# Kernel tuning notes

Hardware: AMD Instinct MI355X
Metric: run time of the kernel (lower is better)

Reference implementation:

```python
import jax, jax.numpy as jnp
import numpy as np

N, C, T, H, W = 4, 512, 8, 28, 28
CQ, CV = C // 8, C // 2  # 64, 256


def _maxpool222(a):
    # max_pool3d with kernel=stride=(2,2,2), VALID, over (t,h,w) of [n,c,t,h,w]
    return jax.lax.reduce_window(a, -jnp.inf, jax.lax.max,
                                 (1, 1, 2, 2, 2), (1, 1, 2, 2, 2), 'VALID')


def setup_inputs() -> dict:
    key = jax.random.key(0)
    ks = jax.random.split(key, 6)
    s = lambda fan_in: 1.0 / np.sqrt(fan_in)
    return {
        'x':  jax.random.normal(ks[0], (N, C, T, H, W), dtype=jnp.float32),
        'Wq': jax.random.normal(ks[1], (CQ, C), dtype=jnp.float32) * s(C),
        'Wk': jax.random.normal(ks[2], (CQ, C), dtype=jnp.float32) * s(C),
        'Wv': jax.random.normal(ks[3], (CV, C), dtype=jnp.float32) * s(C),
        'Wz': jax.random.normal(ks[4], (C, CV), dtype=jnp.float32) * s(CV),
        'y':  jax.random.normal(ks[5], (), dtype=jnp.float32) * 0.1,
    }


def reference(x, Wq, Wk, Wv, Wz, y):
    n, c, t, h, w = x.shape
    # 1x1x1 convs (no bias) = per-voxel channel mixing
    q = jnp.einsum('ncthw,oc->nothw', x, Wq)          # [n, CQ, t, h, w]
    k = _maxpool222(jnp.einsum('ncthw,oc->nothw', x, Wk))  # [n, CQ, t/2, h/2, w/2]
    v = _maxpool222(jnp.einsum('ncthw,oc->nothw', x, Wv))  # [n, CV, t/2, h/2, w/2]

    Lq = t * h * w
    Lk = k.shape[2] * k.shape[3] * k.shape[4]
    qf = q.reshape(n, q.shape[1], Lq)                 # [n, CQ, Lq]
    kf = k.reshape(n, k.shape[1], Lk)                 # [n, CQ, Lk]
    vf = v.reshape(n, v.shape[1], Lk)                 # [n, CV, Lk]

    # beta = softmax(q^T k) over kv axis (NOTE: no 1/sqrt(d) scaling, as in source)
    beta = jax.nn.softmax(jnp.einsum('ncq,nck->nqk', qf, kf), axis=-1)  # [n, Lq, Lk]
    att = jnp.einsum('nck,nqk->ncq', vf, beta)        # [n, CV, Lq]
    att = att.reshape(n, vf.shape[1], t, h, w)

    z = jnp.einsum('ncthw,oc->nothw', att, Wz)        # [n, C, t, h, w]
    return y * z + x
```

## Files before the change

kernel.cpp:

```cpp
#include <hip/hip_runtime.h>
#include <hip/hip_bf16.h>

#define LSP  6272
#define LK   784
#define CIN  512
#define CQo  64
#define CVo  256
#define NB   4

typedef __bf16  bf16x8 __attribute__((ext_vector_type(8)));
typedef __bf16  bf16x4 __attribute__((ext_vector_type(4)));
typedef float   f32x4  __attribute__((ext_vector_type(4)));

#define LDT  40
#define LDS2 72

__global__ __launch_bounds__(256) void xt_kernel(const float* __restrict__ x,
                                                 __bf16* __restrict__ xT)
{
    __shared__ __attribute__((aligned(16))) __bf16 tile[64][68];
    int t = threadIdx.x;
    int p0 = blockIdx.x * 64, c0 = blockIdx.y * 64, n = blockIdx.z;
    #pragma unroll
    for (int i = 0; i < 4; i++) {
        int idx = i * 256 + t;
        int c = idx >> 4, p4 = (idx & 15) * 4;
        const float4 v = *reinterpret_cast<const float4*>(
            &x[((size_t)(n * CIN + c0 + c)) * LSP + p0 + p4]);
        tile[p4 + 0][c] = (__bf16)v.x;
        tile[p4 + 1][c] = (__bf16)v.y;
        tile[p4 + 2][c] = (__bf16)v.z;
        tile[p4 + 3][c] = (__bf16)v.w;
    }
    __syncthreads();
    #pragma unroll
    for (int i = 0; i < 4; i++) {
        int idx = i * 256 + t;
        int p = idx >> 4, c4 = (idx & 15) * 4;
        bf16x4 o;
        o[0] = tile[p][c4 + 0]; o[1] = tile[p][c4 + 1];
        o[2] = tile[p][c4 + 2]; o[3] = tile[p][c4 + 3];
        *reinterpret_cast<bf16x4*>(&xT[((size_t)(n * LSP + p0 + p)) * CIN + c0 + c4]) = o;
    }
}

__global__ void wprep_kernel(const float* __restrict__ Wq, const float* __restrict__ Wk,
                             const float* __restrict__ Wv, const float* __restrict__ Wz,
                             __bf16* __restrict__ Wqkv, __bf16* __restrict__ Wzb)
{
    int idx = blockIdx.x * 256 + threadIdx.x;
    if (idx < 384 * 512) {
        int o = idx >> 9;
        float v = (o < 64) ? Wq[idx] : (o < 128) ? Wk[idx - 64 * 512] : Wv[idx - 128 * 512];
        Wqkv[idx] = (__bf16)v;
    }
    if (idx < 512 * 256) Wzb[idx] = (__bf16)Wz[idx];
}

__global__ __launch_bounds__(256) void qkv_gemm(const __bf16* __restrict__ Wqkv,
                                                const __bf16* __restrict__ xT,
                                                __bf16* __restrict__ qT,
                                                __bf16* __restrict__ kT,
                                                __bf16* __restrict__ vconv)
{
    __shared__ __attribute__((aligned(16))) __bf16 As[128 * LDT];
    __shared__ __attribute__((aligned(16))) __bf16 Bs[128 * LDT];
    int t = threadIdx.x;
    int p0 = blockIdx.x * 128;
    int m0 = blockIdx.y * 128;
    int n  = blockIdx.z;
    int lane = t & 63, wid = t >> 6;
    int wm = wid >> 1, wn = wid & 1;
    int lm = lane & 15, lk = lane >> 4;

    f32x4 acc[4][4] = {};

    for (int kb = 0; kb < CIN; kb += 32) {
        #pragma unroll
        for (int i = 0; i < 2; i++) {
            int idx = i * 2048 + t * 8;
            int r = idx >> 5, k8 = idx & 31;
            uint4 va = *reinterpret_cast<const uint4*>(&Wqkv[(size_t)(m0 + r) * CIN + kb + k8]);
            *reinterpret_cast<uint4*>(&As[r * LDT + k8]) = va;
            uint4 vb = *reinterpret_cast<const uint4*>(&xT[((size_t)(n * LSP + p0 + r)) * CIN + kb + k8]);
            *reinterpret_cast<uint4*>(&Bs[r * LDT + k8]) = vb;
        }
        __syncthreads();
        bf16x8 a[4], b[4];
        #pragma unroll
        for (int mi = 0; mi < 4; mi++)
            a[mi] = *reinterpret_cast<const bf16x8*>(&As[(wm * 64 + mi * 16 + lm) * LDT + lk * 8]);
        #pragma unroll
        for (int ni = 0; ni < 4; ni++)
            b[ni] = *reinterpret_cast<const bf16x8*>(&Bs[(wn * 64 + ni * 16 + lm) * LDT + lk * 8]);
        #pragma unroll
        for (int mi = 0; mi < 4; mi++)
            #pragma unroll
            for (int ni = 0; ni < 4; ni++)
                acc[mi][ni] = __builtin_amdgcn_mfma_f32_16x16x32_bf16(a[mi], b[ni], acc[mi][ni], 0, 0, 0);
        __syncthreads();
    }

    #pragma unroll
    for (int mi = 0; mi < 4; mi++) {
        int mloc = wm * 64 + mi * 16 + lk * 4;
        #pragma unroll
        for (int ni = 0; ni < 4; ni++) {
            int p = p0 + wn * 64 + ni * 16 + lm;
            if (m0 == 0) {
                bf16x4 o;
                o[0] = (__bf16)acc[mi][ni][0]; o[1] = (__bf16)acc[mi][ni][1];
                o[2] = (__bf16)acc[mi][ni][2]; o[3] = (__bf16)acc[mi][ni][3];
                if (mloc < 64)
                    *reinterpret_cast<bf16x4*>(&qT[((size_t)(n * LSP + p)) * 64 + mloc]) = o;
                else
                    *reinterpret_cast<bf16x4*>(&kT[((size_t)(n * LSP + p)) * 64 + (mloc - 64)]) = o;
            } else {
                int cv = m0 - 128 + mloc;
                #pragma unroll
                for (int r = 0; r < 4; r++)
                    vconv[((size_t)(n * CVo + cv + r)) * LSP + p] = (__bf16)acc[mi][ni][r];
            }
        }
    }
}

__global__ __launch_bounds__(256) void poolk_kernel(const __bf16* __restrict__ kT,
                                                    __bf16* __restrict__ kpT)
{
    int wid = threadIdx.x >> 6, lane = threadIdx.x & 63;
    int row = blockIdx.x * 4 + wid;
    int n = row / LK, pk = row % LK;
    int tp = pk / 196, rem = pk % 196, hp = rem / 14, wp = rem % 14;
    const __bf16* b = kT + ((size_t)n * LSP + tp * 2 * 784 + hp * 2 * 28 + wp * 2) * 64 + lane;
    float m =        (float)b[0];
    m = fmaxf(m, (float)b[64]);
    m = fmaxf(m, (float)b[28 * 64]);
    m = fmaxf(m, (float)b[29 * 64]);
    m = fmaxf(m, (float)b[784 * 64]);
    m = fmaxf(m, (float)b[785 * 64]);
    m = fmaxf(m, (float)b[812 * 64]);
    m = fmaxf(m, (float)b[813 * 64]);
    kpT[(size_t)row * 64 + lane] = (__bf16)m;
}

__global__ void poolv_kernel(const __bf16* __restrict__ vconv, __bf16* __restrict__ vp)
{
    int id = blockIdx.x * 256 + threadIdx.x;
    if (id >= NB * CVo * LK) return;
    int nc = id / LK, pk = id % LK;
    int tp = pk / 196, rem = pk % 196, hp = rem / 14, wp = rem % 14;
    const __bf16* b = vconv + (size_t)nc * LSP + tp * 2 * 784 + hp * 2 * 28 + wp * 2;
    float m =        (float)b[0];
    m = fmaxf(m, (float)b[1]);   m = fmaxf(m, (float)b[28]);  m = fmaxf(m, (float)b[29]);
    m = fmaxf(m, (float)b[784]); m = fmaxf(m, (float)b[785]); m = fmaxf(m, (float)b[812]); m = fmaxf(m, (float)b[813]);
    vp[id] = (__bf16)m;
}

__global__ __launch_bounds__(256) void scores_gemm(const __bf16* __restrict__ qT,
                                                   const __bf16* __restrict__ kpT,
                                                   __bf16* __restrict__ sc)
{
    __shared__ __attribute__((aligned(16))) __bf16 As[128 * LDS2];
    __shared__ __attribute__((aligned(16))) __bf16 Bs[128 * LDS2];
    int t = threadIdx.x;
    int k0 = blockIdx.x * 128;
    int q0 = blockIdx.y * 128;
    int n  = blockIdx.z;
    int lane = t & 63, wid = t >> 6;
    int wm = wid >> 1, wn = wid & 1;
    int lm = lane & 15, lk = lane >> 4;

    #pragma unroll
    for (int i = 0; i < 4; i++) {
        int idx = i * 2048 + t * 8;
        int r = idx >> 6, k8 = idx & 63;
        *reinterpret_cast<uint4*>(&As[r * LDS2 + k8]) =
            *reinterpret_cast<const uint4*>(&qT[((size_t)(n * LSP + q0 + r)) * 64 + k8]);
        uint4 vb = {0u, 0u, 0u, 0u};
        if (k0 + r < LK)
            vb = *reinterpret_cast<const uint4*>(&kpT[((size_t)(n * LK + k0 + r)) * 64 + k8]);
        *reinterpret_cast<uint4*>(&Bs[r * LDS2 + k8]) = vb;
    }
    __syncthreads();

    f32x4 acc[4][4] = {};
    #pragma unroll
    for (int ks = 0; ks < 2; ks++) {
        bf16x8 a[4], b[4];
        #pragma unroll
        for (int mi = 0; mi < 4; mi++)
            a[mi] = *reinterpret_cast<const bf16x8*>(&As[(wm * 64 + mi * 16 + lm) * LDS2 + ks * 32 + lk * 8]);
        #pragma unroll
        for (int ni = 0; ni < 4; ni++)
            b[ni] = *reinterpret_cast<const bf16x8*>(&Bs[(wn * 64 + ni * 16 + lm) * LDS2 + ks * 32 + lk * 8]);
        #pragma unroll
        for (int mi = 0; mi < 4; mi++)
            #pragma unroll
            for (int ni = 0; ni < 4; ni++)
                acc[mi][ni] = __builtin_amdgcn_mfma_f32_16x16x32_bf16(a[mi], b[ni], acc[mi][ni], 0, 0, 0);
    }

    #pragma unroll
    for (int mi = 0; mi < 4; mi++) {
        int q = q0 + wm * 64 + mi * 16 + lk * 4;
        #pragma unroll
        for (int ni = 0; ni < 4; ni++) {
            int k = k0 + wn * 64 + ni * 16 + lm;
            if (k < LK) {
                #pragma unroll
                for (int r = 0; r < 4; r++)
                    sc[((size_t)(n * LSP + q + r)) * LK + k] = (__bf16)acc[mi][ni][r];
            }
        }
    }
}

__global__ __launch_bounds__(256) void softmax_kernel(__bf16* __restrict__ sc)
{
    int wid = threadIdx.x >> 6, lane = threadIdx.x & 63;
    size_t row = (size_t)blockIdx.x * 4 + wid;
    __bf16* r = sc + row * LK;
    float v[13];
    float mx = -1e30f;
    #pragma unroll
    for (int i = 0; i < 13; i++) {
        int k = lane + i * 64;
        v[i] = (k < LK) ? (float)r[k] : -1e30f;
        mx = fmaxf(mx, v[i]);
    }
    #pragma unroll
    for (int s = 32; s > 0; s >>= 1) mx = fmaxf(mx, __shfl_xor(mx, s));
    float sum = 0.0f;
    #pragma unroll
    for (int i = 0; i < 13; i++) {
        float e = (lane + i * 64 < LK) ? __expf(v[i] - mx) : 0.0f;
        v[i] = e;
        sum += e;
    }
    #pragma unroll
    for (int s = 32; s > 0; s >>= 1) sum += __shfl_xor(sum, s);
    float inv = 1.0f / sum;
    #pragma unroll
    for (int i = 0; i < 13; i++) {
        int k = lane + i * 64;
        if (k < LK) r[k] = (__bf16)(v[i] * inv);
    }
}

__global__ __launch_bounds__(256) void pv_gemm(const __bf16* __restrict__ vp,
                                               const __bf16* __restrict__ sc,
                                               __bf16* __restrict__ attT)
{
    __shared__ __attribute__((aligned(16))) __bf16 As[128 * LDT];
    __shared__ __attribute__((aligned(16))) __bf16 Bs[128 * LDT];
    int t = threadIdx.x;
    int q0 = blockIdx.x * 128;
    int m0 = blockIdx.y * 128;
    int n  = blockIdx.z;
    int lane = t & 63, wid = t >> 6;
    int wm = wid >> 1, wn = wid & 1;
    int lm = lane & 15, lk = lane >> 4;

    f32x4 acc[4][4] = {};

    for (int kb = 0; kb < 800; kb += 32) {
        #pragma unroll
        for (int i = 0; i < 2; i++) {
            int idx = i * 2048 + t * 8;
            int r = idx >> 5, k8 = idx & 31;
            uint4 va = {0u, 0u, 0u, 0u}, vb = {0u, 0u, 0u, 0u};
            if (kb + k8 < LK) {
                va = *reinterpret_cast<const uint4*>(&vp[((size_t)(n * CVo + m0 + r)) * LK + kb + k8]);
                vb = *reinterpret_cast<const uint4*>(&sc[((size_t)(n * LSP + q0 + r)) * LK + kb + k8]);
            }
            *reinterpret_cast<uint4*>(&As[r * LDT + k8]) = va;
            *reinterpret_cast<uint4*>(&Bs[r * LDT + k8]) = vb;
        }
        __syncthreads();
        bf16x8 a[4], b[4];
        #pragma unroll
        for (int mi = 0; mi < 4; mi++)
            a[mi] = *reinterpret_cast<const bf16x8*>(&As[(wm * 64 + mi * 16 + lm) * LDT + lk * 8]);
        #pragma unroll
        for (int ni = 0; ni < 4; ni++)
            b[ni] = *reinterpret_cast<const bf16x8*>(&Bs[(wn * 64 + ni * 16 + lm) * LDT + lk * 8]);
        #pragma unroll
        for (int mi = 0; mi < 4; mi++)
            #pragma unroll
            for (int ni = 0; ni < 4; ni++)
                acc[mi][ni] = __builtin_amdgcn_mfma_f32_16x16x32_bf16(a[mi], b[ni], acc[mi][ni], 0, 0, 0);
        __syncthreads();
    }

    #pragma unroll
    for (int mi = 0; mi < 4; mi++) {
        int cvb = m0 + wm * 64 + mi * 16 + lk * 4;
        #pragma unroll
        for (int ni = 0; ni < 4; ni++) {
            int q = q0 + wn * 64 + ni * 16 + lm;
            bf16x4 o;
            o[0] = (__bf16)acc[mi][ni][0]; o[1] = (__bf16)acc[mi][ni][1];
            o[2] = (__bf16)acc[mi][ni][2]; o[3] = (__bf16)acc[mi][ni][3];
            *reinterpret_cast<bf16x4*>(&attT[((size_t)(n * LSP + q)) * CVo + cvb]) = o;
        }
    }
}

__global__ __launch_bounds__(256) void z_gemm(const __bf16* __restrict__ Wzb,
                                              const __bf16* __restrict__ attT,
                                              const float* __restrict__ x,
                                              const float* __restrict__ yp,
                                              float* __restrict__ out)
{
    __shared__ __attribute__((aligned(16))) __bf16 As[128 * LDT];
    __shared__ __attribute__((aligned(16))) __bf16 Bs[128 * LDT];
    int t = threadIdx.x;
    int p0 = blockIdx.x * 128;
    int m0 = blockIdx.y * 128;
    int n  = blockIdx.z;
    int lane = t & 63, wid = t >> 6;
    int wm = wid >> 1, wn = wid & 1;
    int lm = lane & 15, lk = lane >> 4;

    f32x4 acc[4][4] = {};

    for (int kb = 0; kb < CVo; kb += 32) {
        #pragma unroll
        for (int i = 0; i < 2; i++) {
            int idx = i * 2048 + t * 8;
            int r = idx >> 5, k8 = idx & 31;
            uint4 va = *reinterpret_cast<const uint4*>(&Wzb[(size_t)(m0 + r) * CVo + kb + k8]);
            *reinterpret_cast<uint4*>(&As[r * LDT + k8]) = va;
            uint4 vb = *reinterpret_cast<const uint4*>(&attT[((size_t)(n * LSP + p0 + r)) * CVo + kb + k8]);
            *reinterpret_cast<uint4*>(&Bs[r * LDT + k8]) = vb;
        }
        __syncthreads();
        bf16x8 a[4], b[4];
        #pragma unroll
        for (int mi = 0; mi < 4; mi++)
            a[mi] = *reinterpret_cast<const bf16x8*>(&As[(wm * 64 + mi * 16 + lm) * LDT + lk * 8]);
        #pragma unroll
        for (int ni = 0; ni < 4; ni++)
            b[ni] = *reinterpret_cast<const bf16x8*>(&Bs[(wn * 64 + ni * 16 + lm) * LDT + lk * 8]);
        #pragma unroll
        for (int mi = 0; mi < 4; mi++)
            #pragma unroll
            for (int ni = 0; ni < 4; ni++)
                acc[mi][ni] = __builtin_amdgcn_mfma_f32_16x16x32_bf16(a[mi], b[ni], acc[mi][ni], 0, 0, 0);
        __syncthreads();
    }

    float yv = yp[0];
    #pragma unroll
    for (int mi = 0; mi < 4; mi++) {
        int c = m0 + wm * 64 + mi * 16 + lk * 4;
        #pragma unroll
        for (int ni = 0; ni < 4; ni++) {
            int p = p0 + wn * 64 + ni * 16 + lm;
            #pragma unroll
            for (int r = 0; r < 4; r++) {
                size_t o = ((size_t)(n * CIN + c + r)) * LSP + p;
                out[o] = yv * acc[mi][ni][r] + x[o];
            }
        }
    }
}

extern "C" void kernel_launch(void* const* d_in, const int* in_sizes, int n_in,
                              void* d_out, int out_size, void* d_ws, size_t ws_size,
                              hipStream_t stream)
{
    const float* x  = (const float*)d_in[0];
    const float* Wq = (const float*)d_in[1];
    const float* Wk = (const float*)d_in[2];
    const float* Wv = (const float*)d_in[3];
    const float* Wz = (const float*)d_in[4];
    const float* y  = (const float*)d_in[5];
    float* out = (float*)d_out;
    __bf16* ws = (__bf16*)d_ws;

    __bf16* xT    = ws;
    __bf16* kT    = ws + (size_t)12845056;
    __bf16* vconv = ws + (size_t)14450688;
    __bf16* sc    = ws;
    __bf16* qT    = ws + (size_t)20873216;
    __bf16* kpT   = ws + (size_t)22478848;
    __bf16* vp    = ws + (size_t)22679552;
    __bf16* attT  = ws + (size_t)23482368;
    __bf16* Wqkv  = ws + (size_t)29904896;
    __bf16* Wzb   = ws + (size_t)30101504;

    xt_kernel   <<<dim3(98, 8, 4), 256, 0, stream>>>(x, xT);
    wprep_kernel<<<dim3(768), 256, 0, stream>>>(Wq, Wk, Wv, Wz, Wqkv, Wzb);
    qkv_gemm    <<<dim3(49, 3, 4), 256, 0, stream>>>(Wqkv, xT, qT, kT, vconv);
    poolk_kernel<<<dim3(784), 256, 0, stream>>>(kT, kpT);
    poolv_kernel<<<dim3(3136), 256, 0, stream>>>(vconv, vp);
    scores_gemm <<<dim3(7, 49, 4), 256, 0, stream>>>(qT, kpT, sc);
    softmax_kernel<<<dim3(6272), 256, 0, stream>>>(sc);
    pv_gemm     <<<dim3(49, 2, 4), 256, 0, stream>>>(vp, sc, attT);
    z_gemm      <<<dim3(49, 4, 4), 256, 0, stream>>>(Wzb, attT, x, y, out);
}
```

Before: 247.4 us.

## Fuse scores, softmax and PV into a flash-attention kernel; vectorize z epilogue

Replaces the separate scores GEMM, softmax pass and PV GEMM with a single online-softmax flash kernel that keeps the probability tile in LDS, so the full 6272x784 score matrix is never written to or re-read from global memory. Each 64-query block streams K and V tiles straight from global memory without LDS staging and rescales its accumulators per tile. The z GEMM operands are also swapped so the epilogue writes float4 along the spatial axis, giving coalesced reads of x and writes of out. The flash grid is small (392 blocks), and the unstaged K/V global loads may limit MFMA throughput.

```diff
diff --git a/kernel.cpp b/kernel.cpp
--- a/kernel.cpp
+++ b/kernel.cpp
@@ -13,7 +13,6 @@
 typedef float   f32x4  __attribute__((ext_vector_type(4)));
 
 #define LDT  40
-#define LDS2 72
 
 __global__ __launch_bounds__(256) void xt_kernel(const float* __restrict__ x,
                                                  __bf16* __restrict__ xT)
@@ -80,10 +79,10 @@
         for (int i = 0; i < 2; i++) {
             int idx = i * 2048 + t * 8;
             int r = idx >> 5, k8 = idx & 31;
-            uint4 va = *reinterpret_cast<const uint4*>(&Wqkv[(size_t)(m0 + r) * CIN + kb + k8]);
-            *reinterpret_cast<uint4*>(&As[r * LDT + k8]) = va;
-            uint4 vb = *reinterpret_cast<const uint4*>(&xT[((size_t)(n * LSP + p0 + r)) * CIN + kb + k8]);
-            *reinterpret_cast<uint4*>(&Bs[r * LDT + k8]) = vb;
+            *reinterpret_cast<uint4*>(&As[r * LDT + k8]) =
+                *reinterpret_cast<const uint4*>(&Wqkv[(size_t)(m0 + r) * CIN + kb + k8]);
+            *reinterpret_cast<uint4*>(&Bs[r * LDT + k8]) =
+                *reinterpret_cast<const uint4*>(&xT[((size_t)(n * LSP + p0 + r)) * CIN + kb + k8]);
         }
         __syncthreads();
         bf16x8 a[4], b[4];
@@ -157,152 +156,131 @@
     vp[id] = (__bf16)m;
 }
 
-__global__ __launch_bounds__(256) void scores_gemm(const __bf16* __restrict__ qT,
-                                                   const __bf16* __restrict__ kpT,
-                                                   __bf16* __restrict__ sc)
-{
-    __shared__ __attribute__((aligned(16))) __bf16 As[128 * LDS2];
-    __shared__ __attribute__((aligned(16))) __bf16 Bs[128 * LDS2];
+__global__ __launch_bounds__(256) void flash_kernel(
+    const __bf16* __restrict__ qT, const __bf16* __restrict__ kpT,
+    const __bf16* __restrict__ vp, __bf16* __restrict__ attT)
+{
+    __shared__ __attribute__((aligned(16))) __bf16 Ps[64 * 128];
+    __shared__ float smem_s[64];
     int t = threadIdx.x;
-    int k0 = blockIdx.x * 128;
-    int q0 = blockIdx.y * 128;
-    int n  = blockIdx.z;
-    int lane = t & 63, wid = t >> 6;
-    int wm = wid >> 1, wn = wid & 1;
+    int lane = t & 63, w = t >> 6;
     int lm = lane & 15, lk = lane >> 4;
-
-    #pragma unroll
-    for (int i = 0; i < 4; i++) {
-        int idx = i * 2048 + t * 8;
-        int r = idx >> 6, k8 = idx & 63;
-        *reinterpret_cast<uint4*>(&As[r * LDS2 + k8]) =
-            *reinterpret_cast<const uint4*>(&qT[((size_t)(n * LSP + q0 + r)) * 64 + k8]);
-        uint4 vb = {0u, 0u, 0u, 0u};
-        if (k0 + r < LK)
-            vb = *reinterpret_cast<const uint4*>(&kpT[((size_t)(n * LK + k0 + r)) * 64 + k8]);
-        *reinterpret_cast<uint4*>(&Bs[r * LDS2 + k8]) = vb;
+    int q0 = blockIdx.x * 64;
+    int n  = blockIdx.y;
+
+    bf16x8 qa[2];
+    {
+        const __bf16* qrow = &qT[((size_t)(n * LSP + q0 + w * 16 + lm)) * 64 + lk * 8];
+        qa[0] = *reinterpret_cast<const bf16x8*>(qrow);
+        qa[1] = *reinterpret_cast<const bf16x8*>(qrow + 32);
+    }
+
+    f32x4 accO[4][4] = {};
+    float m[4], l[4];
+    #pragma unroll
+    for (int r = 0; r < 4; r++) { m[r] = -1e30f; l[r] = 0.0f; }
+
+    int qrow = w * 16 + lk * 4;
+
+    for (int kt = 0; kt < 7; kt++) {
+        int k0 = kt * 128;
+        f32x4 accS[8] = {};
+        #pragma unroll
+        for (int ks = 0; ks < 2; ks++) {
+            #pragma unroll
+            for (int ni = 0; ni < 8; ni++) {
+                int k = k0 + ni * 16 + lm; if (k > 783) k = 783;
+                bf16x8 kb = *reinterpret_cast<const bf16x8*>(
+                    &kpT[((size_t)(n * LK + k)) * 64 + ks * 32 + lk * 8]);
+                accS[ni] = __builtin_amdgcn_mfma_f32_16x16x32_bf16(qa[ks], kb, accS[ni], 0, 0, 0);
+            }
+        }
+        if (kt == 6) {
+            #pragma unroll
+            for (int ni = 1; ni < 8; ni++)
+                #pragma unroll
+                for (int r = 0; r < 4; r++) accS[ni][r] = -1e30f;
+        }
+        float scale[4], lt[4];
+        #pragma unroll
+        for (int r = 0; r < 4; r++) {
+            float v = accS[0][r];
+            #pragma unroll
+            for (int ni = 1; ni < 8; ni++) v = fmaxf(v, accS[ni][r]);
+            #pragma unroll
+            for (int d = 1; d < 16; d <<= 1) v = fmaxf(v, __shfl_xor(v, d));
+            float mn = fmaxf(m[r], v);
+            scale[r] = __expf(m[r] - mn);
+            m[r] = mn;
+            lt[r] = 0.0f;
+        }
+        #pragma unroll
+        for (int ni = 0; ni < 8; ni++)
+            #pragma unroll
+            for (int r = 0; r < 4; r++) {
+                float p = __expf(accS[ni][r] - m[r]);
+                lt[r] += p;
+                int q = qrow + r;
+                int kl = ni * 16 + lm;
+                Ps[q * 128 + (kl ^ ((q & 7) << 3))] = (__bf16)p;
+            }
+        #pragma unroll
+        for (int r = 0; r < 4; r++) {
+            #pragma unroll
+            for (int d = 1; d < 16; d <<= 1) lt[r] += __shfl_xor(lt[r], d);
+            l[r] = l[r] * scale[r] + lt[r];
+        }
+        if (lm == 0) {
+            #pragma unroll
+            for (int r = 0; r < 4; r++) smem_s[qrow + r] = scale[r];
+        }
+        __syncthreads();
+        #pragma unroll
+        for (int ni = 0; ni < 4; ni++) {
+            float s = smem_s[ni * 16 + lm];
+            #pragma unroll
+            for (int mi = 0; mi < 4; mi++)
+                #pragma unroll
+                for (int r = 0; r < 4; r++) accO[mi][ni][r] *= s;
+        }
+        #pragma unroll
+        for (int ks = 0; ks < 4; ks++) {
+            int kg = k0 + ks * 32 + lk * 8; if (kg > 776) kg = 776;
+            bf16x8 pb[4];
+            #pragma unroll
+            for (int ni = 0; ni < 4; ni++) {
+                int q = ni * 16 + lm;
+                pb[ni] = *reinterpret_cast<const bf16x8*>(
+                    &Ps[q * 128 + ((ks * 32 + lk * 8) ^ ((q & 7) << 3))]);
+            }
+            #pragma unroll
+            for (int mi = 0; mi < 4; mi++) {
+                int cv = w * 64 + mi * 16 + lm;
+                bf16x8 va = *reinterpret_cast<const bf16x8*>(
+                    &vp[((size_t)(n * CVo + cv)) * LK + kg]);
+                #pragma unroll
+                for (int ni = 0; ni < 4; ni++)
+                    accO[mi][ni] = __builtin_amdgcn_mfma_f32_16x16x32_bf16(va, pb[ni], accO[mi][ni], 0, 0, 0);
+            }
+        }
+        __syncthreads();
+    }
+    if (lm == 0) {
+        #pragma unroll
+        for (int r = 0; r < 4; r++) smem_s[qrow + r] = 1.0f / l[r];
     }
     __syncthreads();
-
-    f32x4 acc[4][4] = {};
-    #pragma unroll
-    for (int ks = 0; ks < 2; ks++) {
-        bf16x8 a[4], b[4];
-        #pragma unroll
-        for (int mi = 0; mi < 4; mi++)
-            a[mi] = *reinterpret_cast<const bf16x8*>(&As[(wm * 64 + mi * 16 + lm) * LDS2 + ks * 32 + lk * 8]);
-        #pragma unroll
-        for (int ni = 0; ni < 4; ni++)
-            b[ni] = *reinterpret_cast<const bf16x8*>(&Bs[(wn * 64 + ni * 16 + lm) * LDS2 + ks * 32 + lk * 8]);
-        #pragma unroll
-        for (int mi = 0; mi < 4; mi++)
-            #pragma unroll
-            for (int ni = 0; ni < 4; ni++)
-                acc[mi][ni] = __builtin_amdgcn_mfma_f32_16x16x32_bf16(a[mi], b[ni], acc[mi][ni], 0, 0, 0);
-    }
-
-    #pragma unroll
-    for (int mi = 0; mi < 4; mi++) {
-        int q = q0 + wm * 64 + mi * 16 + lk * 4;
-        #pragma unroll
-        for (int ni = 0; ni < 4; ni++) {
-            int k = k0 + wn * 64 + ni * 16 + lm;
-            if (k < LK) {
-                #pragma unroll
-                for (int r = 0; r < 4; r++)
-                    sc[((size_t)(n * LSP + q + r)) * LK + k] = (__bf16)acc[mi][ni][r];
-            }
-        }
-    }
-}
-
-__global__ __launch_bounds__(256) void softmax_kernel(__bf16* __restrict__ sc)
-{
-    int wid = threadIdx.x >> 6, lane = threadIdx.x & 63;
-    size_t row = (size_t)blockIdx.x * 4 + wid;
-    __bf16* r = sc + row * LK;
-    float v[13];
-    float mx = -1e30f;
-    #pragma unroll
-    for (int i = 0; i < 13; i++) {
-        int k = lane + i * 64;
-        v[i] = (k < LK) ? (float)r[k] : -1e30f;
-        mx = fmaxf(mx, v[i]);
-    }
-    #pragma unroll
-    for (int s = 32; s > 0; s >>= 1) mx = fmaxf(mx, __shfl_xor(mx, s));
-    float sum = 0.0f;
-    #pragma unroll
-    for (int i = 0; i < 13; i++) {
-        float e = (lane + i * 64 < LK) ? __expf(v[i] - mx) : 0.0f;
-        v[i] = e;
-        sum += e;
-    }
-    #pragma unroll
-    for (int s = 32; s > 0; s >>= 1) sum += __shfl_xor(sum, s);
-    float inv = 1.0f / sum;
-    #pragma unroll
-    for (int i = 0; i < 13; i++) {
-        int k = lane + i * 64;
-        if (k < LK) r[k] = (__bf16)(v[i] * inv);
-    }
-}
-
-__global__ __launch_bounds__(256) void pv_gemm(const __bf16* __restrict__ vp,
-                                               const __bf16* __restrict__ sc,
-                                               __bf16* __restrict__ attT)
-{
-    __shared__ __attribute__((aligned(16))) __bf16 As[128 * LDT];
-    __shared__ __attribute__((aligned(16))) __bf16 Bs[128 * LDT];
-    int t = threadIdx.x;
-    int q0 = blockIdx.x * 128;
-    int m0 = blockIdx.y * 128;
-    int n  = blockIdx.z;
-    int lane = t & 63, wid = t >> 6;
-    int wm = wid >> 1, wn = wid & 1;
-    int lm = lane & 15, lk = lane >> 4;
-
-    f32x4 acc[4][4] = {};
-
-    for (int kb = 0; kb < 800; kb += 32) {
-        #pragma unroll
-        for (int i = 0; i < 2; i++) {
-            int idx = i * 2048 + t * 8;
-            int r = idx >> 5, k8 = idx & 31;
-            uint4 va = {0u, 0u, 0u, 0u}, vb = {0u, 0u, 0u, 0u};
-            if (kb + k8 < LK) {
-                va = *reinterpret_cast<const uint4*>(&vp[((size_t)(n * CVo + m0 + r)) * LK + kb + k8]);
-                vb = *reinterpret_cast<const uint4*>(&sc[((size_t)(n * LSP + q0 + r)) * LK + kb + k8]);
-            }
-            *reinterpret_cast<uint4*>(&As[r * LDT + k8]) = va;
-            *reinterpret_cast<uint4*>(&Bs[r * LDT + k8]) = vb;
-        }
-        __syncthreads();
-        bf16x8 a[4], b[4];
-        #pragma unroll
-        for (int mi = 0; mi < 4; mi++)
-            a[mi] = *reinterpret_cast<const bf16x8*>(&As[(wm * 64 + mi * 16 + lm) * LDT + lk * 8]);
-        #pragma unroll
-        for (int ni = 0; ni < 4; ni++)
-            b[ni] = *reinterpret_cast<const bf16x8*>(&Bs[(wn * 64 + ni * 16 + lm) * LDT + lk * 8]);
-        #pragma unroll
-        for (int mi = 0; mi < 4; mi++)
-            #pragma unroll
-            for (int ni = 0; ni < 4; ni++)
-                acc[mi][ni] = __builtin_amdgcn_mfma_f32_16x16x32_bf16(a[mi], b[ni], acc[mi][ni], 0, 0, 0);
-        __syncthreads();
-    }
-
-    #pragma unroll
-    for (int mi = 0; mi < 4; mi++) {
-        int cvb = m0 + wm * 64 + mi * 16 + lk * 4;
-        #pragma unroll
-        for (int ni = 0; ni < 4; ni++) {
-            int q = q0 + wn * 64 + ni * 16 + lm;
+    #pragma unroll
+    for (int ni = 0; ni < 4; ni++) {
+        float inv = smem_s[ni * 16 + lm];
+        int q = q0 + ni * 16 + lm;
+        #pragma unroll
+        for (int mi = 0; mi < 4; mi++) {
             bf16x4 o;
-            o[0] = (__bf16)acc[mi][ni][0]; o[1] = (__bf16)acc[mi][ni][1];
-            o[2] = (__bf16)acc[mi][ni][2]; o[3] = (__bf16)acc[mi][ni][3];
-            *reinterpret_cast<bf16x4*>(&attT[((size_t)(n * LSP + q)) * CVo + cvb]) = o;
+            #pragma unroll
+            for (int r = 0; r < 4; r++) o[r] = (__bf16)(accO[mi][ni][r] * inv);
+            *reinterpret_cast<bf16x4*>(
+                &attT[((size_t)(n * LSP + q)) * CVo + w * 64 + mi * 16 + lk * 4]) = o;
         }
     }
 }
@@ -317,7 +295,7 @@
     __shared__ __attribute__((aligned(16))) __bf16 Bs[128 * LDT];
     int t = threadIdx.x;
     int p0 = blockIdx.x * 128;
-    int m0 = blockIdx.y * 128;
+    int c0 = blockIdx.y * 128;
     int n  = blockIdx.z;
     int lane = t & 63, wid = t >> 6;
     int wm = wid >> 1, wn = wid & 1;
@@ -330,10 +308,10 @@
         for (int i = 0; i < 2; i++) {
             int idx = i * 2048 + t * 8;
             int r = idx >> 5, k8 = idx & 31;
-            uint4 va = *reinterpret_cast<const uint4*>(&Wzb[(size_t)(m0 + r) * CVo + kb + k8]);
-            *reinterpret_cast<uint4*>(&As[r * LDT + k8]) = va;
-            uint4 vb = *reinterpret_cast<const uint4*>(&attT[((size_t)(n * LSP + p0 + r)) * CVo + kb + k8]);
-            *reinterpret_cast<uint4*>(&Bs[r * LDT + k8]) = vb;
+            *reinterpret_cast<uint4*>(&As[r * LDT + k8]) =
+                *reinterpret_cast<const uint4*>(&attT[((size_t)(n * LSP + p0 + r)) * CVo + kb + k8]);
+            *reinterpret_cast<uint4*>(&Bs[r * LDT + k8]) =
+                *reinterpret_cast<const uint4*>(&Wzb[(size_t)(c0 + r) * CVo + kb + k8]);
         }
         __syncthreads();
         bf16x8 a[4], b[4];
@@ -354,15 +332,18 @@
     float yv = yp[0];
     #pragma unroll
     for (int mi = 0; mi < 4; mi++) {
-        int c = m0 + wm * 64 + mi * 16 + lk * 4;
+        int p = p0 + wm * 64 + mi * 16 + lk * 4;
         #pragma unroll
         for (int ni = 0; ni < 4; ni++) {
-            int p = p0 + wn * 64 + ni * 16 + lm;
-            #pragma unroll
-            for (int r = 0; r < 4; r++) {
-                size_t o = ((size_t)(n * CIN + c + r)) * LSP + p;
-                out[o] = yv * acc[mi][ni][r] + x[o];
-            }
+            int c = c0 + wn * 64 + ni * 16 + lm;
+            size_t o = ((size_t)(n * CIN + c)) * LSP + p;
+            const float4 xv = *reinterpret_cast<const float4*>(&x[o]);
+            float4 ov;
+            ov.x = yv * acc[mi][ni][0] + xv.x;
+            ov.y = yv * acc[mi][ni][1] + xv.y;
+            ov.z = yv * acc[mi][ni][2] + xv.z;
+            ov.w = yv * acc[mi][ni][3] + xv.w;
+            *reinterpret_cast<float4*>(&out[o]) = ov;
         }
     }
 }
@@ -383,7 +364,6 @@
     __bf16* xT    = ws;
     __bf16* kT    = ws + (size_t)12845056;
     __bf16* vconv = ws + (size_t)14450688;
-    __bf16* sc    = ws;
     __bf16* qT    = ws + (size_t)20873216;
     __bf16* kpT   = ws + (size_t)22478848;
     __bf16* vp    = ws + (size_t)22679552;
@@ -391,13 +371,11 @@
     __bf16* Wqkv  = ws + (size_t)29904896;
     __bf16* Wzb   = ws + (size_t)30101504;
 
-    xt_kernel   <<<dim3(98, 8, 4), 256, 0, stream>>>(x, xT);
-    wprep_kernel<<<dim3(768), 256, 0, stream>>>(Wq, Wk, Wv, Wz, Wqkv, Wzb);
-    qkv_gemm    <<<dim3(49, 3, 4), 256, 0, stream>>>(Wqkv, xT, qT, kT, vconv);
-    poolk_kernel<<<dim3(784), 256, 0, stream>>>(kT, kpT);
-    poolv_kernel<<<dim3(3136), 256, 0, stream>>>(vconv, vp);
-    scores_gemm <<<dim3(7, 49, 4), 256, 0, stream>>>(qT, kpT, sc);
-    softmax_kernel<<<dim3(6272), 256, 0, stream>>>(sc);
-    pv_gemm     <<<dim3(49, 2, 4), 256, 0, stream>>>(vp, sc, attT);
-    z_gemm      <<<dim3(49, 4, 4), 256, 0, stream>>>(Wzb, attT, x, y, out);
-}
+    xt_kernel    <<<dim3(98, 8, 4), 256, 0, stream>>>(x, xT);
+    wprep_kernel <<<dim3(768), 256, 0, stream>>>(Wq, Wk, Wv, Wz, Wqkv, Wzb);
+    qkv_gemm     <<<dim3(49, 3, 4), 256, 0, stream>>>(Wqkv, xT, qT, kT, vconv);
+    poolk_kernel <<<dim3(784), 256, 0, stream>>>(kT, kpT);
+    poolv_kernel <<<dim3(3136), 256, 0, stream>>>(vconv, vp);
+    flash_kernel <<<dim3(98, 4), 256, 0, stream>>>(qT, kpT, vp, attT);
+    z_gemm       <<<dim3(49, 4, 4), 256, 0, stream>>>(Wzb, attT, x, y, out);
+}
```

Measured after the change: 244.9 us. No clear change (-1.0%).
